# Kernel tuning notes

Hardware: AMD Instinct MI355X
Metric: run time of the kernel (lower is better)

The kernel has to match this reference:

```python
import jax, jax.numpy as jnp
import numpy as np

N_FREQ = 256
N_CH = 256
VOCAB = 8192
B, T = 4, 2048


def gauss_proj(x, w, n_freq):
    # FFT over vocab dim, take first n_freq harmonics (skip DC), split real/imag
    X = jnp.fft.rfft(x, axis=-1)[..., 1:n_freq + 1]          # [B,T,n_freq] complex
    X_ri = jnp.concatenate([X.real, X.imag], axis=-1)         # [B,T,2*n_freq]
    return X_ri @ w.T                                         # [B,T,n_channels]


def gauss_synth(h, w, n_freq, V):
    Y_ri = h @ w                                              # [B,T,2*n_freq]
    Y = Y_ri[..., :n_freq] + 1j * Y_ri[..., n_freq:]          # [B,T,n_freq] complex
    full = jnp.zeros(h.shape[:-1] + (V // 2 + 1,), dtype=Y.dtype)
    full = full.at[..., 1:n_freq + 1].set(Y)                  # band-limited spectrum
    return jnp.fft.irfft(full, n=V, axis=-1)                  # [B,T,V]


def setup_inputs() -> dict:
    key = jax.random.key(0)
    ks = jax.random.split(key, 5)
    x = jax.random.normal(ks[0], (B, T, VOCAB), dtype=jnp.float32)
    q_w = jax.random.normal(ks[1], (N_CH, 2 * N_FREQ), dtype=jnp.float32) * 0.02
    k_w = jax.random.normal(ks[2], (N_CH, 2 * N_FREQ), dtype=jnp.float32) * 0.02
    v_w = jax.random.normal(ks[3], (N_CH, 2 * N_FREQ), dtype=jnp.float32) * 0.02
    o_w = jax.random.normal(ks[4], (N_CH, 2 * N_FREQ), dtype=jnp.float32) * 0.02
    decay_logit = jnp.float32(3.0)
    out_scale = jnp.float32(0.1)
    return {"x": x, "q_w": q_w, "k_w": k_w, "v_w": v_w, "o_w": o_w,
            "decay_logit": decay_logit, "out_scale": out_scale}


def reference(x, q_w, k_w, v_w, o_w, decay_logit, out_scale):
    q = gauss_proj(x, q_w, N_FREQ)                            # [B,T,C]
    k = gauss_proj(x, k_w, N_FREQ)
    v = gauss_proj(x, v_w, N_FREQ)
    scores = jnp.einsum('btc,bsc->bts', q, k)                 # [B,T,T]
    decay = jax.nn.sigmoid(decay_logit)
    t = x.shape[1]
    pos = jnp.arange(t)
    # faithful to torch: diff[t,s] = pos[s] - pos[t]
    diff = pos[None, :] - pos[:, None]
    weights = (decay ** jnp.clip(diff.astype(jnp.float32) - 1.0, 0.0)) * (diff > 0)
    scores = scores * weights[None, :, :]
    retrieved = jnp.einsum('bts,bsc->btc', scores, v)         # [B,T,C]
    return gauss_synth(retrieved, o_w, N_FREQ, VOCAB) * out_scale
```

## Files before the change

### kernel.cpp

```cpp
#include <hip/hip_runtime.h>
#include <hip/hip_bf16.h>
#include <cstdint>


typedef unsigned short u16;
typedef short short8 __attribute__((ext_vector_type(8)));
typedef float f32x4 __attribute__((ext_vector_type(4)));
typedef float f4 __attribute__((ext_vector_type(4)));

__device__ __forceinline__ u16 f2bf(float f) {
  union { float f; unsigned u; } v; v.f = f;
  unsigned u = v.u;
  u += 0x7fffu + ((u >> 16) & 1u);
  return (u16)(u >> 16);
}

__device__ __forceinline__ uint2 pack_bf4(f4 v) {
  union { u16 h[4]; uint2 q; } pk;
  pk.h[0] = f2bf(v[0]); pk.h[1] = f2bf(v[1]);
  pk.h[2] = f2bf(v[2]); pk.h[3] = f2bf(v[3]);
  return pk.q;
}

__device__ __forceinline__ void gload_lds16(const void* g, void* l) {
  __builtin_amdgcn_global_load_lds(
      (const __attribute__((address_space(1))) void*)g,
      (__attribute__((address_space(3))) void*)l, 16, 0, 0);
}

__global__ __launch_bounds__(256, 2)
void gemm_g1(const float* __restrict__ A, const u16* __restrict__ B,
             float* __restrict__ P)
{
  constexpr int NN = 512, KK = 8192, KC = 4096;
  constexpr int NT = KC / 64;

  __shared__ u16 As[2][128 * 64] __attribute__((aligned(16)));
  __shared__ u16 Bs[2][128 * 64] __attribute__((aligned(16)));

  const int tid  = threadIdx.x;
  const int wave = tid >> 6, lane = tid & 63;
  const int quad = lane >> 4, l15 = lane & 15;
  const int wm = wave >> 1, wn = wave & 1;
  const int swz8 = (l15 & 7) << 3;

  const int lid = blockIdx.x;
  const int nat = (lid & 7) * 64 + (lid >> 3);
  const int y = nat >> 3, rem = nat & 7;
  const int x = rem & 3, z = rem >> 2;
  const int m0 = y * 128, n0 = x * 128, k00 = z * KC;

  const int brow = tid >> 3;
  const int bswz = ((tid & 7) * 8) ^ (((tid >> 3) & 7) << 3);
  const u16* Bp = B + (size_t)(n0 + brow) * KK + k00 + bswz;
  const int bloff = tid * 16;

  const int arow16 = tid >> 4;
  const int acolf  = (tid & 15) * 4;
  const float* Ap = A + (size_t)(m0 + arow16) * KK + k00 + acolf;
  const int awz = ((tid & 15) * 4) ^ (((tid >> 4) & 7) << 3);

  f4 rv0[8], rv1[8];

#define ISSUE_A(RV, T)                                               \
  _Pragma("unroll")                                                  \
  for (int g = 0; g < 8; ++g)                                        \
    RV[g] = *(const f4*)(Ap + (size_t)g * 16 * KK + (size_t)(T) * 64);
#define ISSUE_B(T, SLOT)                                             \
  _Pragma("unroll")                                                  \
  for (int h = 0; h < 4; ++h)                                        \
    gload_lds16(Bp + (size_t)h * 32 * KK + (size_t)(T) * 64,         \
                (char*)Bs[SLOT] + h * 4096 + bloff);
#define CONVERT_A(RV, SLOT)                                          \
  _Pragma("unroll")                                                  \
  for (int g = 0; g < 8; ++g)                                        \
    *(uint2*)&As[SLOT][(g * 16 + arow16) * 64 + awz] = pack_bf4(RV[g]);
#define G1_COMPUTE(CUR)                                                          \
  _Pragma("unroll")                                                              \
  for (int ks = 0; ks < 2; ++ks) {                                               \
    short8 a[4], b[4];                                                           \
    _Pragma("unroll")                                                            \
    for (int i = 0; i < 4; ++i)                                                  \
      a[i] = *(const short8*)&As[CUR][(wm * 64 + i * 16 + l15) * 64 +            \
                                      ((ks * 32 + quad * 8) ^ swz8)];            \
    _Pragma("unroll")                                                            \
    for (int j = 0; j < 4; ++j)                                                  \
      b[j] = *(const short8*)&Bs[CUR][(wn * 64 + j * 16 + l15) * 64 +            \
                                      ((ks * 32 + quad * 8) ^ swz8)];            \
    _Pragma("unroll")                                                            \
    for (int i = 0; i < 4; ++i)                                                  \
      _Pragma("unroll")                                                          \
      for (int j = 0; j < 4; ++j)                                                \
        acc[i][j] = __builtin_amdgcn_mfma_f32_16x16x32_bf16(a[i], b[j], acc[i][j], 0, 0, 0); \
  }
#define SB() __builtin_amdgcn_sched_barrier(0)
#define FENCE_BAR()                                                  \
  asm volatile("s_waitcnt vmcnt(8)" ::: "memory");                   \
  asm volatile("s_waitcnt lgkmcnt(0)" ::: "memory");                 \
  __builtin_amdgcn_s_barrier();                                      \
  asm volatile("" ::: "memory");

  ISSUE_A(rv0, 0);
  ISSUE_B(0, 0);
  SB();
  ISSUE_A(rv1, 1);
  SB();
  CONVERT_A(rv0, 0);
  FENCE_BAR();

  f32x4 acc[4][4] = {};

#define BODY(T, RV_ISS, RV_CONV)                                     \
  {                                                                  \
    const int t2 = ((T) + 2 < NT) ? (T) + 2 : NT - 1;                \
    ISSUE_B((T) + 1 < NT ? (T) + 1 : NT - 1, ((T) + 1) & 1);         \
    SB();                                                            \
    ISSUE_A(RV_ISS, t2);                                             \
    SB();                                                            \
    G1_COMPUTE((T) & 1);                                             \
    CONVERT_A(RV_CONV, ((T) + 1) & 1);                               \
    FENCE_BAR();                                                     \
  }

  for (int t = 0; t < NT; t += 2) {
    BODY(t, rv0, rv1);
    BODY(t + 1, rv1, rv0);
  }
#undef BODY
#undef FENCE_BAR
#undef SB
#undef G1_COMPUTE
#undef CONVERT_A
#undef ISSUE_B
#undef ISSUE_A

  float* Pz = P + (size_t)z * (8192L * 512);
  #pragma unroll
  for (int i = 0; i < 4; ++i) {
    #pragma unroll
    for (int j = 0; j < 4; ++j) {
      const int rb = m0 + wm * 64 + i * 16 + quad * 4;
      const int cc = n0 + wn * 64 + j * 16 + l15;
      #pragma unroll
      for (int r = 0; r < 4; ++r)
        Pz[(size_t)(rb + r) * NN + cc] = acc[i][j][r];
    }
  }
}

__global__ void reduce_cast(const float* __restrict__ P, u16* __restrict__ O,
                            int half_f4) {
  const int i = blockIdx.x * 256 + threadIdx.x;
  const f4 a = ((const f4*)P)[i];
  const f4 b = ((const f4*)P)[i + half_f4];
  union { u16 h[4]; uint2 q; } pk;
  #pragma unroll
  for (int r = 0; r < 4; ++r) pk.h[r] = f2bf(a[r] + b[r]);
  ((uint2*)O)[i] = pk.q;
}

__global__ __launch_bounds__(256, 2)
void gemm_qkvw(const u16* __restrict__ Xri, const u16* __restrict__ Fm,
               const u16* __restrict__ qwb, const u16* __restrict__ kwb,
               const u16* __restrict__ vwb, const u16* __restrict__ owb,
               u16* __restrict__ Qb, u16* __restrict__ Kb,
               u16* __restrict__ Vt, u16* __restrict__ Wot)
{
  constexpr int N = 256, K = 512;
  __shared__ u16 As[128 * 32] __attribute__((aligned(16)));
  __shared__ u16 Bs[128 * 32] __attribute__((aligned(16)));

  const int tid  = threadIdx.x;
  const int wave = tid >> 6, lane = tid & 63;
  const int quad = lane >> 4, l15 = lane & 15;
  const int wm = wave >> 1, wn = wave & 1;
  const int m0 = blockIdx.y * 128, n0 = blockIdx.x * 128;
  const int z  = blockIdx.z;

  const u16* Ab = (z == 3) ? Fm : Xri;
  const u16* Bb = (z == 0) ? qwb : (z == 1) ? kwb : (z == 2) ? vwb : owb;
  const float alpha = (z == 3) ? (2.f / 8192.f) : 1.f;

  f32x4 acc[4][4] = {};

  const int loff0 = wave * 2048 + lane * 16;
  const int loff1 = loff0 + 1024;
  const int row0s = loff0 >> 6, kof0 = (loff0 & 63) >> 1;
  const int row1s = loff1 >> 6, kof1 = (loff1 & 63) >> 1;

  for (int k0 = 0; k0 < K; k0 += 32) {
    __syncthreads();
    gload_lds16(Ab + (size_t)(m0 + row0s) * K + k0 + kof0, (char*)As + loff0);
    gload_lds16(Ab + (size_t)(m0 + row1s) * K + k0 + kof1, (char*)As + loff1);
    gload_lds16(Bb + (size_t)(n0 + row0s) * K + k0 + kof0, (char*)Bs + loff0);
    gload_lds16(Bb + (size_t)(n0 + row1s) * K + k0 + kof1, (char*)Bs + loff1);
    __syncthreads();

    short8 a[4], b[4];
    #pragma unroll
    for (int i = 0; i < 4; ++i)
      a[i] = *(const short8*)&As[(wm * 64 + i * 16 + l15) * 32 + quad * 8];
    #pragma unroll
    for (int j = 0; j < 4; ++j)
      b[j] = *(const short8*)&Bs[(wn * 64 + j * 16 + l15) * 32 + quad * 8];
    #pragma unroll
    for (int i = 0; i < 4; ++i)
      #pragma unroll
      for (int j = 0; j < 4; ++j)
        acc[i][j] = __builtin_amdgcn_mfma_f32_16x16x32_bf16(a[i], b[j], acc[i][j], 0, 0, 0);
  }

  #pragma unroll
  for (int i = 0; i < 4; ++i) {
    #pragma unroll
    for (int j = 0; j < 4; ++j) {
      f32x4 v = acc[i][j];
      const int rb = m0 + wm * 64 + i * 16 + quad * 4;
      const int cc = n0 + wn * 64 + j * 16 + l15;
      if (z == 2) {
        const int bb = rb >> 11, ml = rb & 2047;
        union { u16 h[4]; uint2 q; } pk;
        #pragma unroll
        for (int r = 0; r < 4; ++r) pk.h[r] = f2bf(v[r]);
        *(uint2*)&Vt[((size_t)(bb << 8) + cc) * 2048 + ml] = pk.q;
      } else {
        u16* C = (z == 0) ? Qb : (z == 1) ? Kb : Wot;
        #pragma unroll
        for (int r = 0; r < 4; ++r)
          C[(size_t)(rb + r) * N + cc] = f2bf(v[r] * alpha);
      }
    }
  }
}

__global__ __launch_bounds__(256, 2)
void gemm_g5(const u16* __restrict__ S, const u16* __restrict__ Vt,
             float* __restrict__ P5)
{
  constexpr int N = 256, K = 2048;
  __shared__ u16 As[128 * 32] __attribute__((aligned(16)));
  __shared__ u16 Bs[128 * 32] __attribute__((aligned(16)));

  const int tid  = threadIdx.x;
  const int wave = tid >> 6, lane = tid & 63;
  const int quad = lane >> 4, l15 = lane & 15;
  const int wm = wave >> 1, wn = wave & 1;
  const int m0 = blockIdx.y * 128, n0 = blockIdx.x * 128;
  const int batch = blockIdx.z & 3, half = blockIdx.z >> 2;

  const u16* Ab = S  + (size_t)batch * 2048 * 2048;
  const u16* Bb = Vt + (size_t)batch * 256 * 2048;

  int kbeg = half * 1024;
  if (m0 > kbeg) kbeg = m0;
  const int kend = half * 1024 + 1024;

  f32x4 acc[4][4] = {};

  const int loff0 = wave * 2048 + lane * 16;
  const int loff1 = loff0 + 1024;
  const int row0s = loff0 >> 6, kof0 = (loff0 & 63) >> 1;
  const int row1s = loff1 >> 6, kof1 = (loff1 & 63) >> 1;

  for (int k0 = kbeg; k0 < kend; k0 += 32) {
    __syncthreads();
    gload_lds16(Ab + (size_t)(m0 + row0s) * K + k0 + kof0, (char*)As + loff0);
    gload_lds16(Ab + (size_t)(m0 + row1s) * K + k0 + kof1, (char*)As + loff1);
    gload_lds16(Bb + (size_t)(n0 + row0s) * K + k0 + kof0, (char*)Bs + loff0);
    gload_lds16(Bb + (size_t)(n0 + row1s) * K + k0 + kof1, (char*)Bs + loff1);
    __syncthreads();

    short8 a[4], b[4];
    #pragma unroll
    for (int i = 0; i < 4; ++i)
      a[i] = *(const short8*)&As[(wm * 64 + i * 16 + l15) * 32 + quad * 8];
    #pragma unroll
    for (int j = 0; j < 4; ++j)
      b[j] = *(const short8*)&Bs[(wn * 64 + j * 16 + l15) * 32 + quad * 8];
    #pragma unroll
    for (int i = 0; i < 4; ++i)
      #pragma unroll
      for (int j = 0; j < 4; ++j)
        acc[i][j] = __builtin_amdgcn_mfma_f32_16x16x32_bf16(a[i], b[j], acc[i][j], 0, 0, 0);
  }

  float* Pz = P5 + (size_t)half * (8192L * 256) + (size_t)batch * 2048 * 256;
  #pragma unroll
  for (int i = 0; i < 4; ++i) {
    #pragma unroll
    for (int j = 0; j < 4; ++j) {
      const int rb = m0 + wm * 64 + i * 16 + quad * 4;
      const int cc = n0 + wn * 64 + j * 16 + l15;
      #pragma unroll
      for (int r = 0; r < 4; ++r)
        Pz[(size_t)(rb + r) * N + cc] = acc[i][j][r];
    }
  }
}

template<int EPI, bool AF32, bool TRI>
__global__ __launch_bounds__(256, 2)
void gemm_bt(const void* __restrict__ Av, const u16* __restrict__ B,
             void* __restrict__ Cv, int M, int N, int K,
             long sA, long sB, long sC,
             const float* __restrict__ scal, float alpha)
{
  if (TRI && blockIdx.x < blockIdx.y) return;

  __shared__ u16 As[128 * 32] __attribute__((aligned(16)));
  __shared__ u16 Bs[128 * 32] __attribute__((aligned(16)));

  const int tid  = threadIdx.x;
  const int wave = tid >> 6, lane = tid & 63;
  const int quad = lane >> 4, l15 = lane & 15;
  const int wm = wave >> 1, wn = wave & 1;
  const int m0 = blockIdx.y * 128, n0 = blockIdx.x * 128;
  const int z  = blockIdx.z;

  const u16*   Ab = (const u16*)Av + (size_t)z * sA;
  const float* Af = (const float*)Av + (size_t)z * sA;
  const u16*   Bb = B + (size_t)z * sB;

  f32x4 acc[4][4] = {};

  const int loff0 = wave * 2048 + lane * 16;
  const int loff1 = loff0 + 1024;
  const int row0s = loff0 >> 6, kof0 = (loff0 & 63) >> 1;
  const int row1s = loff1 >> 6, kof1 = (loff1 & 63) >> 1;

  for (int k0 = 0; k0 < K; k0 += 32) {
    __syncthreads();
    if (AF32) {
      const int row = tid >> 1, half = tid & 1;
      const float* ar = Af + (size_t)(m0 + row) * K + k0 + half * 16;
      f4 p0 = *(const f4*)(ar);
      f4 p1 = *(const f4*)(ar + 4);
      f4 p2 = *(const f4*)(ar + 8);
      f4 p3 = *(const f4*)(ar + 12);
      union { u16 h[16]; uint4 q[2]; } pk;
      #pragma unroll
      for (int e = 0; e < 4; ++e) {
        pk.h[e]      = f2bf(p0[e]);
        pk.h[4 + e]  = f2bf(p1[e]);
        pk.h[8 + e]  = f2bf(p2[e]);
        pk.h[12 + e] = f2bf(p3[e]);
      }
      uint4* dst = (uint4*)&As[row * 32 + half * 16];
      dst[0] = pk.q[0]; dst[1] = pk.q[1];
    } else {
      gload_lds16(Ab + (size_t)(m0 + row0s) * K + k0 + kof0, (char*)As + loff0);
      gload_lds16(Ab + (size_t)(m0 + row1s) * K + k0 + kof1, (char*)As + loff1);
    }
    gload_lds16(Bb + (size_t)(n0 + row0s) * K + k0 + kof0, (char*)Bs + loff0);
    gload_lds16(Bb + (size_t)(n0 + row1s) * K + k0 + kof1, (char*)Bs + loff1);
    __syncthreads();

    short8 a[4], b[4];
    #pragma unroll
    for (int i = 0; i < 4; ++i)
      a[i] = *(const short8*)&As[(wm * 64 + i * 16 + l15) * 32 + quad * 8];
    #pragma unroll
    for (int j = 0; j < 4; ++j)
      b[j] = *(const short8*)&Bs[(wn * 64 + j * 16 + l15) * 32 + quad * 8];
    #pragma unroll
    for (int i = 0; i < 4; ++i)
      #pragma unroll
      for (int j = 0; j < 4; ++j)
        acc[i][j] = __builtin_amdgcn_mfma_f32_16x16x32_bf16(a[i], b[j], acc[i][j], 0, 0, 0);
  }

  float dec_l2 = 0.f, oscale = 1.f;
  if (EPI == 3) {
    float logit = *scal;
    float dec = 1.f / (1.f + expf(-logit));
    dec_l2 = log2f(dec);
  }
  if (EPI == 4) oscale = *scal;

  #pragma unroll
  for (int i = 0; i < 4; ++i) {
    #pragma unroll
    for (int j = 0; j < 4; ++j) {
      f32x4 v = acc[i][j];
      const int rb = m0 + wm * 64 + i * 16 + quad * 4;
      const int cc = n0 + wn * 64 + j * 16 + l15;
      if (EPI == 0) {
        u16* C = (u16*)Cv + (size_t)z * sC;
        #pragma unroll
        for (int r = 0; r < 4; ++r)
          C[(size_t)(rb + r) * N + cc] = f2bf(v[r] * alpha);
      } else if (EPI == 3) {
        u16* C = (u16*)Cv + (size_t)z * sC;
        #pragma unroll
        for (int r = 0; r < 4; ++r) {
          const int d = cc - (rb + r);
          float w = (d > 0) ? exp2f(dec_l2 * (float)(d - 1)) : 0.f;
          C[(size_t)(rb + r) * N + cc] = f2bf(v[r] * w);
        }
      } else if (EPI == 4) {
        float* C = (float*)Cv;
        #pragma unroll
        for (int r = 0; r < 4; ++r)
          C[(size_t)(rb + r) * N + cc] = v[r] * oscale;
      }
    }
  }
}

__global__ void genF_row(u16* Fm) {
  int idx = blockIdx.x * 256 + threadIdx.x;
  int n = idx >> 9, j = idx & 511;
  int k = (j & 255) + 1;
  int ph = (n * k) & 8191;
  float ang = (float)ph * 7.66990393942820795e-4f;
  float s, c; sincosf(ang, &s, &c);
  Fm[idx] = f2bf(j < 256 ? c : -s);
}
__global__ void genF_col(u16* Ft) {
  int idx = blockIdx.x * 256 + threadIdx.x;
  int j = idx >> 13, n = idx & 8191;
  int k = (j & 255) + 1;
  int ph = (n * k) & 8191;
  float ang = (float)ph * 7.66990393942820795e-4f;
  float s, c; sincosf(ang, &s, &c);
  Ft[idx] = f2bf(j < 256 ? c : -s);
}

__global__ void cast_w4(const float* a, const float* b, const float* c, const float* d,
                        u16* oa, u16* ob, u16* oc, u16* od) {
  int i = blockIdx.x * 256 + threadIdx.x;
  oa[i] = f2bf(a[i]); ob[i] = f2bf(b[i]); oc[i] = f2bf(c[i]); od[i] = f2bf(d[i]);
}

extern "C" void kernel_launch(void* const* d_in, const int* in_sizes, int n_in,
                              void* d_out, int out_size, void* d_ws, size_t ws_size,
                              hipStream_t stream)
{
  const float* x  = (const float*)d_in[0];
  const float* qw = (const float*)d_in[1];
  const float* kw = (const float*)d_in[2];
  const float* vw = (const float*)d_in[3];
  const float* ow = (const float*)d_in[4];
  const float* dl = (const float*)d_in[5];
  const float* os = (const float*)d_in[6];
  float* out = (float*)d_out;

  char* W = (char*)d_ws;
  const size_t MB = 1024 * 1024;
  u16* Fm  = (u16*)(W);
  u16* Ft  = (u16*)(W + 8 * MB);
  u16* Xri = (u16*)(W + 16 * MB);
  u16* Qb  = (u16*)(W + 24 * MB);
  u16* Kb  = (u16*)(W + 28 * MB);
  u16* Vt  = (u16*)(W + 32 * MB);
  u16* Wot = (u16*)(W + 36 * MB);
  u16* S   = (u16*)(W + 40 * MB);
  float* P = (float*)(W + 40 * MB);
  float* P5 = (float*)(W);
  u16* R   = (u16*)(W + 72 * MB);
  u16* qwb = (u16*)(W + 76 * MB);
  u16* kwb = qwb + 131072;
  u16* vwb = kwb + 131072;
  u16* owb = vwb + 131072;

  genF_row<<<8192 * 512 / 256, 256, 0, stream>>>(Fm);
  genF_col<<<8192 * 512 / 256, 256, 0, stream>>>(Ft);
  cast_w4<<<131072 / 256, 256, 0, stream>>>(qw, kw, vw, ow, qwb, kwb, vwb, owb);

  gemm_g1<<<512, 256, 0, stream>>>(x, Ft, P);
  reduce_cast<<<4096, 256, 0, stream>>>(P, Xri, 8192 * 512 / 4);

  gemm_qkvw<<<dim3(2, 64, 4), 256, 0, stream>>>(Xri, Fm, qwb, kwb, vwb, owb,
                                                Qb, Kb, Vt, Wot);

  gemm_bt<3, false, true><<<dim3(16, 16, 4), 256, 0, stream>>>(Qb, Kb, S, 2048, 2048, 256,
                                                               2048L * 256, 2048L * 256, 2048L * 2048, dl, 1.f);
  gemm_g5<<<dim3(2, 16, 8), 256, 0, stream>>>(S, Vt, P5);
  reduce_cast<<<2048, 256, 0, stream>>>(P5, R, 8192 * 256 / 4);

  gemm_bt<4, false, false><<<dim3(64, 64, 1), 256, 0, stream>>>(R, Wot, out, 8192, 8192, 256, 0, 0, 0, os, 1.f);
}
```

Baseline: 624.5 us.

## Double-buffer LDS with BK=64 and XOR swizzle in shared GEMM k-loop

Adds a common k-loop helper that stages 64-wide K tiles into two LDS buffers, prefetching the next tile while MFMAs consume the current one, with one barrier per step instead of two. The LDS layout is XOR-swizzled to avoid bank conflicts on the short8 reads. The qkvw, scores, S·V and output GEMMs all use it, and the templated gemm_bt becomes dedicated kernels. LDS per block grows to 64 KB, which may limit occupancy under launch_bounds(256,2). The helper is also skipped when the causal k-range is empty.

```diff
diff --git a/kernel.cpp b/kernel.cpp
--- a/kernel.cpp
+++ b/kernel.cpp
@@ -159,6 +159,64 @@
   ((uint2*)O)[i] = pk.q;
 }
 
+__device__ __forceinline__ void kloop_p(
+    const u16* __restrict__ Ab, const u16* __restrict__ Bb, int K,
+    int m0, int n0, int kbeg, int kend, int tid,
+    u16* As, u16* Bs, f32x4 (&acc)[4][4])
+{
+  const int wave = tid >> 6, lane = tid & 63;
+  const int quad = lane >> 4, l15 = lane & 15;
+  const int wm = wave >> 1, wn = wave & 1;
+  const int swz8 = (l15 & 7) << 3;
+
+  const int brow = tid >> 3;
+  const int rswz = ((tid & 7) * 8) ^ ((brow & 7) << 3);
+  const u16* Apg = Ab + (size_t)(m0 + brow) * K + rswz;
+  const u16* Bpg = Bb + (size_t)(n0 + brow) * K + rswz;
+  const int dof = tid * 16;
+
+#define STG_P(K0, SLOT)                                                     \
+  _Pragma("unroll")                                                         \
+  for (int h = 0; h < 4; ++h) {                                             \
+    gload_lds16(Apg + (size_t)h * 32 * K + (K0),                            \
+                (char*)As + (SLOT) * 16384 + h * 4096 + dof);               \
+    gload_lds16(Bpg + (size_t)h * 32 * K + (K0),                            \
+                (char*)Bs + (SLOT) * 16384 + h * 4096 + dof);               \
+  }
+
+  STG_P(kbeg, 0);
+  asm volatile("s_waitcnt vmcnt(0)" ::: "memory");
+  __builtin_amdgcn_s_barrier();
+  asm volatile("" ::: "memory");
+
+  int buf = 0;
+  for (int k0 = kbeg; k0 < kend; k0 += 64) {
+    if (k0 + 64 < kend) STG_P(k0 + 64, buf ^ 1);
+    #pragma unroll
+    for (int ks = 0; ks < 2; ++ks) {
+      short8 a[4], b[4];
+      #pragma unroll
+      for (int i = 0; i < 4; ++i)
+        a[i] = *(const short8*)&As[buf * 8192 + (wm * 64 + i * 16 + l15) * 64 +
+                                   ((ks * 32 + quad * 8) ^ swz8)];
+      #pragma unroll
+      for (int j = 0; j < 4; ++j)
+        b[j] = *(const short8*)&Bs[buf * 8192 + (wn * 64 + j * 16 + l15) * 64 +
+                                   ((ks * 32 + quad * 8) ^ swz8)];
+      #pragma unroll
+      for (int i = 0; i < 4; ++i)
+        #pragma unroll
+        for (int j = 0; j < 4; ++j)
+          acc[i][j] = __builtin_amdgcn_mfma_f32_16x16x32_bf16(a[i], b[j], acc[i][j], 0, 0, 0);
+    }
+    asm volatile("s_waitcnt vmcnt(0)" ::: "memory");
+    __builtin_amdgcn_s_barrier();
+    asm volatile("" ::: "memory");
+    buf ^= 1;
+  }
+#undef STG_P
+}
+
 __global__ __launch_bounds__(256, 2)
 void gemm_qkvw(const u16* __restrict__ Xri, const u16* __restrict__ Fm,
                const u16* __restrict__ qwb, const u16* __restrict__ kwb,
@@ -167,8 +225,8 @@
                u16* __restrict__ Vt, u16* __restrict__ Wot)
 {
   constexpr int N = 256, K = 512;
-  __shared__ u16 As[128 * 32] __attribute__((aligned(16)));
-  __shared__ u16 Bs[128 * 32] __attribute__((aligned(16)));
+  __shared__ u16 As[2 * 128 * 64] __attribute__((aligned(16)));
+  __shared__ u16 Bs[2 * 128 * 64] __attribute__((aligned(16)));
 
   const int tid  = threadIdx.x;
   const int wave = tid >> 6, lane = tid & 63;
@@ -182,33 +240,7 @@
   const float alpha = (z == 3) ? (2.f / 8192.f) : 1.f;
 
   f32x4 acc[4][4] = {};
-
-  const int loff0 = wave * 2048 + lane * 16;
-  const int loff1 = loff0 + 1024;
-  const int row0s = loff0 >> 6, kof0 = (loff0 & 63) >> 1;
-  const int row1s = loff1 >> 6, kof1 = (loff1 & 63) >> 1;
-
-  for (int k0 = 0; k0 < K; k0 += 32) {
-    __syncthreads();
-    gload_lds16(Ab + (size_t)(m0 + row0s) * K + k0 + kof0, (char*)As + loff0);
-    gload_lds16(Ab + (size_t)(m0 + row1s) * K + k0 + kof1, (char*)As + loff1);
-    gload_lds16(Bb + (size_t)(n0 + row0s) * K + k0 + kof0, (char*)Bs + loff0);
-    gload_lds16(Bb + (size_t)(n0 + row1s) * K + k0 + kof1, (char*)Bs + loff1);
-    __syncthreads();
-
-    short8 a[4], b[4];
-    #pragma unroll
-    for (int i = 0; i < 4; ++i)
-      a[i] = *(const short8*)&As[(wm * 64 + i * 16 + l15) * 32 + quad * 8];
-    #pragma unroll
-    for (int j = 0; j < 4; ++j)
-      b[j] = *(const short8*)&Bs[(wn * 64 + j * 16 + l15) * 32 + quad * 8];
-    #pragma unroll
-    for (int i = 0; i < 4; ++i)
-      #pragma unroll
-      for (int j = 0; j < 4; ++j)
-        acc[i][j] = __builtin_amdgcn_mfma_f32_16x16x32_bf16(a[i], b[j], acc[i][j], 0, 0, 0);
-  }
+  kloop_p(Ab, Bb, K, m0, n0, 0, K, tid, As, Bs, acc);
 
   #pragma unroll
   for (int i = 0; i < 4; ++i) {
@@ -234,81 +266,13 @@
 }
 
 __global__ __launch_bounds__(256, 2)
-void gemm_g5(const u16* __restrict__ S, const u16* __restrict__ Vt,
-             float* __restrict__ P5)
-{
-  constexpr int N = 256, K = 2048;
-  __shared__ u16 As[128 * 32] __attribute__((aligned(16)));
-  __shared__ u16 Bs[128 * 32] __attribute__((aligned(16)));
-
-  const int tid  = threadIdx.x;
-  const int wave = tid >> 6, lane = tid & 63;
-  const int quad = lane >> 4, l15 = lane & 15;
-  const int wm = wave >> 1, wn = wave & 1;
-  const int m0 = blockIdx.y * 128, n0 = blockIdx.x * 128;
-  const int batch = blockIdx.z & 3, half = blockIdx.z >> 2;
-
-  const u16* Ab = S  + (size_t)batch * 2048 * 2048;
-  const u16* Bb = Vt + (size_t)batch * 256 * 2048;
-
-  int kbeg = half * 1024;
-  if (m0 > kbeg) kbeg = m0;
-  const int kend = half * 1024 + 1024;
-
-  f32x4 acc[4][4] = {};
-
-  const int loff0 = wave * 2048 + lane * 16;
-  const int loff1 = loff0 + 1024;
-  const int row0s = loff0 >> 6, kof0 = (loff0 & 63) >> 1;
-  const int row1s = loff1 >> 6, kof1 = (loff1 & 63) >> 1;
-
-  for (int k0 = kbeg; k0 < kend; k0 += 32) {
-    __syncthreads();
-    gload_lds16(Ab + (size_t)(m0 + row0s) * K + k0 + kof0, (char*)As + loff0);
-    gload_lds16(Ab + (size_t)(m0 + row1s) * K + k0 + kof1, (char*)As + loff1);
-    gload_lds16(Bb + (size_t)(n0 + row0s) * K + k0 + kof0, (char*)Bs + loff0);
-    gload_lds16(Bb + (size_t)(n0 + row1s) * K + k0 + kof1, (char*)Bs + loff1);
-    __syncthreads();
-
-    short8 a[4], b[4];
-    #pragma unroll
-    for (int i = 0; i < 4; ++i)
-      a[i] = *(const short8*)&As[(wm * 64 + i * 16 + l15) * 32 + quad * 8];
-    #pragma unroll
-    for (int j = 0; j < 4; ++j)
-      b[j] = *(const short8*)&Bs[(wn * 64 + j * 16 + l15) * 32 + quad * 8];
-    #pragma unroll
-    for (int i = 0; i < 4; ++i)
-      #pragma unroll
-      for (int j = 0; j < 4; ++j)
-        acc[i][j] = __builtin_amdgcn_mfma_f32_16x16x32_bf16(a[i], b[j], acc[i][j], 0, 0, 0);
-  }
-
-  float* Pz = P5 + (size_t)half * (8192L * 256) + (size_t)batch * 2048 * 256;
-  #pragma unroll
-  for (int i = 0; i < 4; ++i) {
-    #pragma unroll
-    for (int j = 0; j < 4; ++j) {
-      const int rb = m0 + wm * 64 + i * 16 + quad * 4;
-      const int cc = n0 + wn * 64 + j * 16 + l15;
-      #pragma unroll
-      for (int r = 0; r < 4; ++r)
-        Pz[(size_t)(rb + r) * N + cc] = acc[i][j][r];
-    }
-  }
-}
-
-template<int EPI, bool AF32, bool TRI>
-__global__ __launch_bounds__(256, 2)
-void gemm_bt(const void* __restrict__ Av, const u16* __restrict__ B,
-             void* __restrict__ Cv, int M, int N, int K,
-             long sA, long sB, long sC,
-             const float* __restrict__ scal, float alpha)
-{
-  if (TRI && blockIdx.x < blockIdx.y) return;
-
-  __shared__ u16 As[128 * 32] __attribute__((aligned(16)));
-  __shared__ u16 Bs[128 * 32] __attribute__((aligned(16)));
+void gemm_g4(const u16* __restrict__ Qb, const u16* __restrict__ Kb,
+             u16* __restrict__ S, const float* __restrict__ dl)
+{
+  if (blockIdx.x < blockIdx.y) return;
+  constexpr int N = 2048, K = 256;
+  __shared__ u16 As[2 * 128 * 64] __attribute__((aligned(16)));
+  __shared__ u16 Bs[2 * 128 * 64] __attribute__((aligned(16)));
 
   const int tid  = threadIdx.x;
   const int wave = tid >> 6, lane = tid & 63;
@@ -317,65 +281,16 @@
   const int m0 = blockIdx.y * 128, n0 = blockIdx.x * 128;
   const int z  = blockIdx.z;
 
-  const u16*   Ab = (const u16*)Av + (size_t)z * sA;
-  const float* Af = (const float*)Av + (size_t)z * sA;
-  const u16*   Bb = B + (size_t)z * sB;
+  const u16* Ab = Qb + (size_t)z * 2048 * 256;
+  const u16* Bb = Kb + (size_t)z * 2048 * 256;
 
   f32x4 acc[4][4] = {};
-
-  const int loff0 = wave * 2048 + lane * 16;
-  const int loff1 = loff0 + 1024;
-  const int row0s = loff0 >> 6, kof0 = (loff0 & 63) >> 1;
-  const int row1s = loff1 >> 6, kof1 = (loff1 & 63) >> 1;
-
-  for (int k0 = 0; k0 < K; k0 += 32) {
-    __syncthreads();
-    if (AF32) {
-      const int row = tid >> 1, half = tid & 1;
-      const float* ar = Af + (size_t)(m0 + row) * K + k0 + half * 16;
-      f4 p0 = *(const f4*)(ar);
-      f4 p1 = *(const f4*)(ar + 4);
-      f4 p2 = *(const f4*)(ar + 8);
-      f4 p3 = *(const f4*)(ar + 12);
-      union { u16 h[16]; uint4 q[2]; } pk;
-      #pragma unroll
-      for (int e = 0; e < 4; ++e) {
-        pk.h[e]      = f2bf(p0[e]);
-        pk.h[4 + e]  = f2bf(p1[e]);
-        pk.h[8 + e]  = f2bf(p2[e]);
-        pk.h[12 + e] = f2bf(p3[e]);
-      }
-      uint4* dst = (uint4*)&As[row * 32 + half * 16];
-      dst[0] = pk.q[0]; dst[1] = pk.q[1];
-    } else {
-      gload_lds16(Ab + (size_t)(m0 + row0s) * K + k0 + kof0, (char*)As + loff0);
-      gload_lds16(Ab + (size_t)(m0 + row1s) * K + k0 + kof1, (char*)As + loff1);
-    }
-    gload_lds16(Bb + (size_t)(n0 + row0s) * K + k0 + kof0, (char*)Bs + loff0);
-    gload_lds16(Bb + (size_t)(n0 + row1s) * K + k0 + kof1, (char*)Bs + loff1);
-    __syncthreads();
-
-    short8 a[4], b[4];
-    #pragma unroll
-    for (int i = 0; i < 4; ++i)
-      a[i] = *(const short8*)&As[(wm * 64 + i * 16 + l15) * 32 + quad * 8];
-    #pragma unroll
-    for (int j = 0; j < 4; ++j)
-      b[j] = *(const short8*)&Bs[(wn * 64 + j * 16 + l15) * 32 + quad * 8];
-    #pragma unroll
-    for (int i = 0; i < 4; ++i)
-      #pragma unroll
-      for (int j = 0; j < 4; ++j)
-        acc[i][j] = __builtin_amdgcn_mfma_f32_16x16x32_bf16(a[i], b[j], acc[i][j], 0, 0, 0);
-  }
-
-  float dec_l2 = 0.f, oscale = 1.f;
-  if (EPI == 3) {
-    float logit = *scal;
-    float dec = 1.f / (1.f + expf(-logit));
-    dec_l2 = log2f(dec);
-  }
-  if (EPI == 4) oscale = *scal;
+  kloop_p(Ab, Bb, K, m0, n0, 0, K, tid, As, Bs, acc);
+
+  const float logit = *dl;
+  const float dec = 1.f / (1.f + expf(-logit));
+  const float dec_l2 = log2f(dec);
+  u16* C = S + (size_t)z * 2048 * 2048;
 
   #pragma unroll
   for (int i = 0; i < 4; ++i) {
@@ -384,25 +299,83 @@
       f32x4 v = acc[i][j];
       const int rb = m0 + wm * 64 + i * 16 + quad * 4;
       const int cc = n0 + wn * 64 + j * 16 + l15;
-      if (EPI == 0) {
-        u16* C = (u16*)Cv + (size_t)z * sC;
-        #pragma unroll
-        for (int r = 0; r < 4; ++r)
-          C[(size_t)(rb + r) * N + cc] = f2bf(v[r] * alpha);
-      } else if (EPI == 3) {
-        u16* C = (u16*)Cv + (size_t)z * sC;
-        #pragma unroll
-        for (int r = 0; r < 4; ++r) {
-          const int d = cc - (rb + r);
-          float w = (d > 0) ? exp2f(dec_l2 * (float)(d - 1)) : 0.f;
-          C[(size_t)(rb + r) * N + cc] = f2bf(v[r] * w);
-        }
-      } else if (EPI == 4) {
-        float* C = (float*)Cv;
-        #pragma unroll
-        for (int r = 0; r < 4; ++r)
-          C[(size_t)(rb + r) * N + cc] = v[r] * oscale;
+      #pragma unroll
+      for (int r = 0; r < 4; ++r) {
+        const int d = cc - (rb + r);
+        float w = (d > 0) ? exp2f(dec_l2 * (float)(d - 1)) : 0.f;
+        C[(size_t)(rb + r) * N + cc] = f2bf(v[r] * w);
       }
+    }
+  }
+}
+
+__global__ __launch_bounds__(256, 2)
+void gemm_g5(const u16* __restrict__ S, const u16* __restrict__ Vt,
+             float* __restrict__ P5)
+{
+  constexpr int N = 256, K = 2048;
+  __shared__ u16 As[2 * 128 * 64] __attribute__((aligned(16)));
+  __shared__ u16 Bs[2 * 128 * 64] __attribute__((aligned(16)));
+
+  const int tid  = threadIdx.x;
+  const int wave = tid >> 6, lane = tid & 63;
+  const int quad = lane >> 4, l15 = lane & 15;
+  const int wm = wave >> 1, wn = wave & 1;
+  const int m0 = blockIdx.y * 128, n0 = blockIdx.x * 128;
+  const int batch = blockIdx.z & 3, half = blockIdx.z >> 2;
+
+  const u16* Ab = S  + (size_t)batch * 2048 * 2048;
+  const u16* Bb = Vt + (size_t)batch * 256 * 2048;
+
+  int kbeg = half * 1024;
+  if (m0 > kbeg) kbeg = m0;
+  const int kend = half * 1024 + 1024;
+
+  f32x4 acc[4][4] = {};
+  if (kbeg < kend)
+    kloop_p(Ab, Bb, K, m0, n0, kbeg, kend, tid, As, Bs, acc);
+
+  float* Pz = P5 + (size_t)half * (8192L * 256) + (size_t)batch * 2048 * 256;
+  #pragma unroll
+  for (int i = 0; i < 4; ++i) {
+    #pragma unroll
+    for (int j = 0; j < 4; ++j) {
+      const int rb = m0 + wm * 64 + i * 16 + quad * 4;
+      const int cc = n0 + wn * 64 + j * 16 + l15;
+      #pragma unroll
+      for (int r = 0; r < 4; ++r)
+        Pz[(size_t)(rb + r) * N + cc] = acc[i][j][r];
+    }
+  }
+}
+
+__global__ __launch_bounds__(256, 2)
+void gemm_g6(const u16* __restrict__ R, const u16* __restrict__ Wot,
+             float* __restrict__ out, const float* __restrict__ os)
+{
+  constexpr int N = 8192, K = 256;
+  __shared__ u16 As[2 * 128 * 64] __attribute__((aligned(16)));
+  __shared__ u16 Bs[2 * 128 * 64] __attribute__((aligned(16)));
+
+  const int tid  = threadIdx.x;
+  const int wave = tid >> 6, lane = tid & 63;
+  const int quad = lane >> 4, l15 = lane & 15;
+  const int wm = wave >> 1, wn = wave & 1;
+  const int m0 = blockIdx.y * 128, n0 = blockIdx.x * 128;
+
+  f32x4 acc[4][4] = {};
+  kloop_p(R, Wot, K, m0, n0, 0, K, tid, As, Bs, acc);
+
+  const float oscale = *os;
+  #pragma unroll
+  for (int i = 0; i < 4; ++i) {
+    #pragma unroll
+    for (int j = 0; j < 4; ++j) {
+      const int rb = m0 + wm * 64 + i * 16 + quad * 4;
+      const int cc = n0 + wn * 64 + j * 16 + l15;
+      #pragma unroll
+      for (int r = 0; r < 4; ++r)
+        out[(size_t)(rb + r) * N + cc] = acc[i][j][r] * oscale;
     }
   }
 }
@@ -473,10 +446,10 @@
   gemm_qkvw<<<dim3(2, 64, 4), 256, 0, stream>>>(Xri, Fm, qwb, kwb, vwb, owb,
                                                 Qb, Kb, Vt, Wot);
 
-  gemm_bt<3, false, true><<<dim3(16, 16, 4), 256, 0, stream>>>(Qb, Kb, S, 2048, 2048, 256,
-                                                               2048L * 256, 2048L * 256, 2048L * 2048, dl, 1.f);
+  gemm_g4<<<dim3(16, 16, 4), 256, 0, stream>>>(Qb, Kb, S, dl);
+
   gemm_g5<<<dim3(2, 16, 8), 256, 0, stream>>>(S, Vt, P5);
   reduce_cast<<<2048, 256, 0, stream>>>(P5, R, 8192 * 256 / 4);
 
-  gemm_bt<4, false, false><<<dim3(64, 64, 1), 256, 0, stream>>>(R, Wot, out, 8192, 8192, 256, 0, 0, 0, os, 1.f);
-}
+  gemm_g6<<<dim3(64, 64, 1), 256, 0, stream>>>(R, Wot, out, os);
+}
```

New measurement: 622.6 us. About the same (-0.3%).
